# Optimization experiments

Hardware: AMD Instinct MI355X
Metric: run time of the kernel (lower is better)

Reference implementation:

```python
import jax, jax.numpy as jnp
import numpy as np

B, C, H, W = 64, 128, 56, 56
ALPHA = 0.001


def _build_inhi_mat(out_channels):
    # Circulant 0/1 band: row i has ones at columns (i-r//2 ... i+r//2) mod C,
    # exactly matching the torch double loop with modular wrap-around.
    r = out_channels // 8 + 1  # inhiRange
    i = np.arange(out_channels)[:, None]
    d = np.arange(-(r // 2), r // 2 + 1)[None, :]
    cols = (i + d) % out_channels  # [C, r]
    m = np.zeros((out_channels, out_channels), dtype=np.float32)
    m[np.repeat(i, d.shape[1], axis=1), cols] = 1.0
    return m


def setup_inputs() -> dict:
    key = jax.random.key(0)
    x = jax.random.normal(key, (B, C, H, W), dtype=jnp.float32)
    inhiMat = jnp.asarray(_build_inhi_mat(C))  # [C, C] constant buffer
    return {"x": x, "inhiMat": inhiMat}


def reference(x, inhiMat):
    b, c, h, w = x.shape
    inhiRange = c // 8 + 1
    # y = detach(x)^2 -> banded cross-channel sum (bmm with broadcast [C,C] mat)
    y = jax.lax.stop_gradient(x) ** 2
    y = y.reshape(b, c, h * w)
    y = jnp.einsum('ij,bjs->bis', inhiMat, y)  # same math as bmm with tiled inhi
    y = y.reshape(b, c, h, w)
    denom = (y * ALPHA / inhiRange + 1.0) ** 0.75
    return x / denom
```

## Files before the change

### kernel.cpp

```cpp
#include <hip/hip_runtime.h>


#define B_DIM 64
#define C_DIM 128
#define HW_DIM (56 * 56)
#define HW2 (HW_DIM / 2)
#define NCOL2 (B_DIM * HW2)
#define NSEG 4
#define SEGC (C_DIM / NSEG)
#define PLANES (SEGC + 16)

__device__ __forceinline__ float pow_m075(float t) {
    return __builtin_amdgcn_exp2f(-0.75f * __builtin_amdgcn_logf(t));
}

__global__ __launch_bounds__(64, 3) void lrn_kernel(const float2* __restrict__ x,
                                                    float2* __restrict__ out) {
    const float kAlphaOverR = 0.001f / 17.0f;

    const int col = blockIdx.x * 64 + threadIdx.x;
    const int b   = col / HW2;
    const int hw2 = col - b * HW2;
    const int c0  = blockIdx.y * SEGC;

    const float2* base = x + ((size_t)b * C_DIM) * HW2 + hw2;
    float2* obase      = out + ((size_t)b * C_DIM) * HW2 + hw2;

    float2 v[PLANES];
#pragma unroll
    for (int j = 0; j < PLANES; ++j) {
        const int ch = (c0 + j - 8 + C_DIM) & (C_DIM - 1);
        v[j] = base[(size_t)ch * HW2];
    }
    __builtin_amdgcn_sched_barrier(0);

    float sx = 0.f, sy = 0.f;
#pragma unroll
    for (int j = 0; j < 17; ++j) {
        sx = fmaf(v[j].x, v[j].x, sx);
        sy = fmaf(v[j].y, v[j].y, sy);
    }

#pragma unroll
    for (int i = 0; i < SEGC; ++i) {
        const float2 xc = v[8 + i];
        float2 o;
        o.x = xc.x * pow_m075(fmaf(sx, kAlphaOverR, 1.0f));
        o.y = xc.y * pow_m075(fmaf(sy, kAlphaOverR, 1.0f));
        obase[(size_t)(c0 + i) * HW2] = o;

        if (i < SEGC - 1) {
            const float2 a = v[17 + i];
            const float2 d = v[i];
            sx += a.x * a.x - d.x * d.x;
            sy += a.y * a.y - d.y * d.y;
        }
    }
}

extern "C" void kernel_launch(void* const* d_in, const int* in_sizes, int n_in,
                              void* d_out, int out_size, void* d_ws, size_t ws_size,
                              hipStream_t stream) {
    const float2* x = (const float2*)d_in[0];
    float2* out = (float2*)d_out;

    dim3 grid(NCOL2 / 64, NSEG);
    lrn_kernel<<<grid, 64, 0, stream>>>(x, out);
}
```

Before: 185.7 us.

## Stream channel planes through a register ring buffer and enlarge thread blocks

Each thread no longer preloads all 48 channel planes. A 19-entry register ring is filled with a two-plane lookahead and refilled as the sliding-window sum advances, which cuts register pressure. Block size grows from 64 to 256 threads with launch bounds of 6 blocks per CU, and the scheduling barrier is removed. The aim is higher occupancy to hide memory latency, at the cost of fewer loads in flight per thread.

New measurement: 207.2 us. 1.12x slower.

```diff
diff --git a/kernel.cpp b/kernel.cpp
--- a/kernel.cpp
+++ b/kernel.cpp
@@ -1,60 +1,63 @@
 #include <hip/hip_runtime.h>
 
 
-#define B_DIM 64
-#define C_DIM 128
-#define HW_DIM (56 * 56)
-#define HW2 (HW_DIM / 2)
-#define NCOL2 (B_DIM * HW2)
+#define HW2 1568
+#define BSTR (128 * HW2)
+#define NCOL2 (64 * HW2)
 #define NSEG 4
-#define SEGC (C_DIM / NSEG)
-#define PLANES (SEGC + 16)
+#define SEGC (128 / NSEG)
+#define RINGN 19
+#define LA 2
 
 __device__ __forceinline__ float pow_m075(float t) {
     return __builtin_amdgcn_exp2f(-0.75f * __builtin_amdgcn_logf(t));
 }
 
-__global__ __launch_bounds__(64, 3) void lrn_kernel(const float2* __restrict__ x,
-                                                    float2* __restrict__ out) {
+__global__ __launch_bounds__(256, 6) void lrn_kernel(const float2* __restrict__ x,
+                                                     float2* __restrict__ out) {
     const float kAlphaOverR = 0.001f / 17.0f;
 
-    const int col = blockIdx.x * 64 + threadIdx.x;
+    const int col = blockIdx.x * 256 + threadIdx.x;
     const int b   = col / HW2;
     const int hw2 = col - b * HW2;
     const int c0  = blockIdx.y * SEGC;
 
-    const float2* base = x + ((size_t)b * C_DIM) * HW2 + hw2;
-    float2* obase      = out + ((size_t)b * C_DIM) * HW2 + hw2;
+    const float2* base = x + (size_t)b * BSTR + hw2;
+    float2* obase      = out + (size_t)b * BSTR + hw2;
 
-    float2 v[PLANES];
+    float2 r[RINGN];
 #pragma unroll
-    for (int j = 0; j < PLANES; ++j) {
-        const int ch = (c0 + j - 8 + C_DIM) & (C_DIM - 1);
-        v[j] = base[(size_t)ch * HW2];
+    for (int p = -8; p <= 8 + LA; ++p) {
+        const int ch = (c0 + p) & 127;
+        r[p + 8] = base[(size_t)ch * HW2];
     }
-    __builtin_amdgcn_sched_barrier(0);
 
     float sx = 0.f, sy = 0.f;
 #pragma unroll
     for (int j = 0; j < 17; ++j) {
-        sx = fmaf(v[j].x, v[j].x, sx);
-        sy = fmaf(v[j].y, v[j].y, sy);
+        sx = fmaf(r[j].x, r[j].x, sx);
+        sy = fmaf(r[j].y, r[j].y, sy);
     }
 
 #pragma unroll
     for (int i = 0; i < SEGC; ++i) {
-        const float2 xc = v[8 + i];
+        const int s_out = i % RINGN;
+        const float2 vout = r[s_out];
+
+        if (i + 9 + LA <= SEGC + 7) {
+            const int ch = (c0 + i + 9 + LA) & 127;
+            r[s_out] = base[(size_t)ch * HW2];
+        }
+
+        const float2 xc = r[(i + 8) % RINGN];
         float2 o;
         o.x = xc.x * pow_m075(fmaf(sx, kAlphaOverR, 1.0f));
         o.y = xc.y * pow_m075(fmaf(sy, kAlphaOverR, 1.0f));
         obase[(size_t)(c0 + i) * HW2] = o;
 
-        if (i < SEGC - 1) {
-            const float2 a = v[17 + i];
-            const float2 d = v[i];
-            sx += a.x * a.x - d.x * d.x;
-            sy += a.y * a.y - d.y * d.y;
-        }
+        const float2 a = r[(i + 17) % RINGN];
+        sx += a.x * a.x - vout.x * vout.x;
+        sy += a.y * a.y - vout.y * vout.y;
     }
 }
 
@@ -64,6 +67,6 @@
     const float2* x = (const float2*)d_in[0];
     float2* out = (float2*)d_out;
 
-    dim3 grid(NCOL2 / 64, NSEG);
-    lrn_kernel<<<grid, 64, 0, stream>>>(x, out);
+    dim3 grid(NCOL2 / 256, NSEG);
+    lrn_kernel<<<grid, 256, 0, stream>>>(x, out);
 }
```
